# Optimization experiments

Measured on AMD Instinct MI355X. Metric: run time of the kernel, lower is better.

Reference implementation:

```python
import jax, jax.numpy as jnp
import numpy as np

N = 100000   # nodes
E = 1600000  # edges
DIM = 64
DIMS = [128, 64, 64, 64]  # [2*DIM] + 3*[DIM]
MAX_DEG = 64
NUM_LAB = 16

def _leaky(x):
    return jnp.where(x >= 0, x, 0.01 * x)

def _bn(x, g, b, eps=1e-5):
    # BatchNorm1d in training mode: per-feature batch mean / biased variance
    m = x.mean(axis=0)
    v = x.var(axis=0)
    return (x - m) * jax.lax.rsqrt(v + eps) * g + b

def setup_inputs() -> dict:
    key = jax.random.key(0)
    ks = jax.random.split(key, 40)
    d = {}
    d["node_deg"] = jax.random.randint(ks[0], (N,), 0, MAX_DEG + 1)
    d["node_lab"] = jax.random.randint(ks[1], (N,), 0, NUM_LAB)
    d["edge_index"] = jax.random.randint(ks[2], (2, E), 0, N)
    d["emb_deg"] = jax.random.normal(ks[3], (MAX_DEG + 1, DIM), jnp.float32) * 0.1
    d["emb_lab"] = jax.random.normal(ks[4], (NUM_LAB, DIM), jnp.float32) * 0.1
    k = 5
    for i, (n1, n2) in enumerate(zip(DIMS[:-1], DIMS[1:])):
        d[f"w{i}"] = jax.random.normal(ks[k], (n2, n1), jnp.float32) / np.sqrt(n1); k += 1
        d[f"b{i}"] = jnp.zeros((n2,), jnp.float32)
        d[f"g{i}"] = jnp.ones((n2,), jnp.float32)
        d[f"be{i}"] = jnp.zeros((n2,), jnp.float32)
    SUMD = sum(DIMS)  # 320
    d["fw1"] = jax.random.normal(ks[k], (DIM, SUMD), jnp.float32) / np.sqrt(SUMD); k += 1
    d["fb1"] = jnp.zeros((DIM,), jnp.float32)
    d["fg"] = jnp.ones((DIM,), jnp.float32)
    d["fbe"] = jnp.zeros((DIM,), jnp.float32)
    d["fw2"] = jax.random.normal(ks[k], (1, DIM), jnp.float32) / np.sqrt(DIM)
    d["fb2"] = jnp.zeros((1,), jnp.float32)
    return d

def reference(node_deg, node_lab, edge_index, emb_deg, emb_lab,
              w0, b0, g0, be0, w1, b1, g1, be1, w2, b2, g2, be2,
              fw1, fb1, fg, fbe, fw2, fb2):
    src, dst = edge_index[0], edge_index[1]
    # input embedding: concat of degree and label embeddings -> [N, 128]
    x0 = jnp.concatenate([emb_deg[node_deg], emb_lab[node_lab]], axis=1)
    z = [x0]
    for (w, b, g, be) in [(w0, b0, g0, be0), (w1, b1, g1, be1), (w2, b2, g2, be2)]:
        x = z[-1]
        # GINConv (eps=0): h = Linear(x + sum_{j in N(i)} x_j)
        agg = jax.ops.segment_sum(x[src], dst, num_segments=N)
        h = (x + agg) @ w.T + b
        z.append(_leaky(_bn(h, g, be)))
    xc = jnp.concatenate(z, axis=1)  # [N, 320]
    h = _leaky(_bn(xc @ fw1.T + fb1, fg, fbe))
    return jax.nn.sigmoid(h @ fw2.T + fb2).squeeze()  # [N]
```

## Files before the change

kernel.cpp:

```cpp
#include <hip/hip_runtime.h>
#include <math.h>

typedef __bf16 bf16;
typedef __attribute__((ext_vector_type(8))) __bf16 bf16x8;
typedef __attribute__((ext_vector_type(4))) float f32x4;

#define NBLK 128
#define NB_MAX 1600

__device__ __forceinline__ void bn_coeffs(const float* st, const float* g,
                                          const float* be, float inv_n, int d,
                                          float& sc, float& sh) {
  float mean = st[d] * inv_n;
  float var = st[64 + d] * inv_n - mean * mean;
  sc = g[d] * rsqrtf(var + 1e-5f);
  sh = be[d] - mean * sc;
}

__global__ __launch_bounds__(256) void bin_hist_kernel(const int* __restrict__ dst,
                                                       int* __restrict__ cnt,
                                                       int E, int ch, int nb) {
  __shared__ int lcnt[NB_MAX];
  int tid = threadIdx.x, blk = blockIdx.x;
  for (int t = tid; t < nb; t += 256) lcnt[t] = 0;
  __syncthreads();
  int base = blk * ch, eend = min(E, base + ch);
  for (int e = base + tid; e < eend; e += 256) atomicAdd(&lcnt[dst[e] >> 6], 1);
  __syncthreads();
  for (int t = tid; t < nb; t += 256) cnt[blk * nb + t] = lcnt[t];
}

__global__ __launch_bounds__(256) void bin_tot_kernel(const int* __restrict__ cnt,
                                                      int* __restrict__ tot, int nb) {
  int b = blockIdx.x * 256 + threadIdx.x;
  if (b >= nb) return;
  int s = 0;
  for (int blk = 0; blk < NBLK; ++blk) s += cnt[blk * nb + b];
  tot[b] = s;
}

__global__ __launch_bounds__(256) void scan_buckets_kernel(const int* __restrict__ tot,
                                                           int* __restrict__ bucketptr, int nb) {
  __shared__ int lds[256];
  int tid = threadIdx.x;
  const int CH = 7;
  int vals[CH];
  int s = 0;
#pragma unroll
  for (int k = 0; k < CH; ++k) {
    int i = tid * CH + k;
    vals[k] = (i < nb) ? tot[i] : 0;
    s += vals[k];
  }
  lds[tid] = s;
  __syncthreads();
  for (int off = 1; off < 256; off <<= 1) {
    int v = (tid >= off) ? lds[tid - off] : 0;
    __syncthreads();
    lds[tid] += v;
    __syncthreads();
  }
  int run = lds[tid] - s;
  if (tid == 0) bucketptr[0] = 0;
#pragma unroll
  for (int k = 0; k < CH; ++k) {
    int i = tid * CH + k;
    run += vals[k];
    if (i < nb) bucketptr[i + 1] = run;
  }
}

__global__ __launch_bounds__(256) void bin_off_kernel(const int* __restrict__ cnt,
                                                      const int* __restrict__ bucketptr,
                                                      int* __restrict__ woff, int nb) {
  int b = blockIdx.x * 256 + threadIdx.x;
  if (b >= nb) return;
  int run = bucketptr[b];
  for (int blk = 0; blk < NBLK; ++blk) {
    woff[blk * nb + b] = run;
    run += cnt[blk * nb + b];
  }
}

__global__ __launch_bounds__(256) void bin_scatter_kernel(const int* __restrict__ src,
                                                          const int* __restrict__ dst,
                                                          const int* __restrict__ woff,
                                                          int* __restrict__ packed,
                                                          int E, int ch, int nb) {
  __shared__ int cur[NB_MAX];
  int tid = threadIdx.x, blk = blockIdx.x;
  for (int t = tid; t < nb; t += 256) cur[t] = woff[blk * nb + t];
  __syncthreads();
  int base = blk * ch, eend = min(E, base + ch);
  for (int e = base + tid; e < eend; e += 256) {
    int d = dst[e], s = src[e];
    int pos = atomicAdd(&cur[d >> 6], 1);
    packed[pos] = ((d & 63) << 17) | s;
  }
}

__global__ __launch_bounds__(256) void csr_finalize_kernel(
    const int* __restrict__ packed, const int* __restrict__ bucketptr,
    int* __restrict__ rowptr, int* __restrict__ colidx, int n, int E) {
  __shared__ int hist[64], offs[64];
  int tid = threadIdx.x, b = blockIdx.x;
  if (tid < 64) hist[tid] = 0;
  __syncthreads();
  int beg = bucketptr[b], end = bucketptr[b + 1];
  for (int e = beg + tid; e < end; e += 256) atomicAdd(&hist[packed[e] >> 17], 1);
  __syncthreads();
  if (tid == 0) {
    int run = 0;
    for (int j = 0; j < 64; ++j) { offs[j] = run; run += hist[j]; }
  }
  __syncthreads();
  if (tid < 64) {
    int idx = b * 64 + tid;
    if (idx < n) rowptr[idx] = beg + offs[tid];
    hist[tid] = offs[tid];
  }
  if (b == 0 && tid == 64) rowptr[n] = E;
  __syncthreads();
  for (int e = beg + tid; e < end; e += 256) {
    int w = packed[e];
    int pos = atomicAdd(&hist[w >> 17], 1);
    colidx[beg + pos] = w & 0x1FFFF;
  }
}

__global__ __launch_bounds__(256) void mfma_gemm0(
    const int* __restrict__ deg, const int* __restrict__ lab,
    const float* __restrict__ ed, const float* __restrict__ el,
    const float* __restrict__ W, bf16* __restrict__ y, int n) {
  __shared__ bf16 As[64][136];
  __shared__ bf16 Bs[64][136];
  int tid = threadIdx.x;
  int nbase = blockIdx.x * 64;
  {
    int r = tid >> 2, c = tid & 3;
    int node = nbase + r;
    union { bf16 hh[32]; uint4 u[4]; } t;
    if (node < n) {
      int idx = (c < 2) ? deg[node] : lab[node];
      const float* srcp = (c < 2) ? (ed + (size_t)idx * 64 + c * 32)
                                  : (el + (size_t)idx * 64 + (c - 2) * 32);
#pragma unroll
      for (int j = 0; j < 8; ++j) {
        float4 f = ((const float4*)srcp)[j];
        t.hh[j * 4 + 0] = (bf16)f.x; t.hh[j * 4 + 1] = (bf16)f.y;
        t.hh[j * 4 + 2] = (bf16)f.z; t.hh[j * 4 + 3] = (bf16)f.w;
      }
    } else {
#pragma unroll
      for (int j = 0; j < 4; ++j) t.u[j] = uint4{0, 0, 0, 0};
    }
#pragma unroll
    for (int j = 0; j < 4; ++j) *(uint4*)&As[r][c * 32 + j * 8] = t.u[j];
    const float4* wp = (const float4*)(W + r * 128 + c * 32);
#pragma unroll
    for (int j = 0; j < 4; ++j) {
      float4 f0 = wp[j * 2], f1 = wp[j * 2 + 1];
      union { bf16 h[8]; uint4 u; } tw;
      tw.h[0] = (bf16)f0.x; tw.h[1] = (bf16)f0.y; tw.h[2] = (bf16)f0.z; tw.h[3] = (bf16)f0.w;
      tw.h[4] = (bf16)f1.x; tw.h[5] = (bf16)f1.y; tw.h[6] = (bf16)f1.z; tw.h[7] = (bf16)f1.w;
      *(uint4*)&Bs[r][c * 32 + j * 8] = tw.u;
    }
  }
  __syncthreads();
  int l = tid & 63, w = tid >> 6, m = l & 15, quad = l >> 4;
  f32x4 acc[4] = {{0.f, 0.f, 0.f, 0.f}, {0.f, 0.f, 0.f, 0.f},
                  {0.f, 0.f, 0.f, 0.f}, {0.f, 0.f, 0.f, 0.f}};
#pragma unroll
  for (int k0 = 0; k0 < 128; k0 += 32) {
    bf16x8 a = *(const bf16x8*)&As[w * 16 + m][k0 + quad * 8];
#pragma unroll
    for (int t = 0; t < 4; ++t) {
      bf16x8 b = *(const bf16x8*)&Bs[t * 16 + m][k0 + quad * 8];
      acc[t] = __builtin_amdgcn_mfma_f32_16x16x32_bf16(a, b, acc[t], 0, 0, 0);
    }
  }
#pragma unroll
  for (int t = 0; t < 4; ++t)
#pragma unroll
    for (int r4 = 0; r4 < 4; ++r4) {
      int node = nbase + w * 16 + quad * 4 + r4;
      if (node < n) y[(size_t)node * 64 + t * 16 + m] = (bf16)acc[t][r4];
    }
}

__global__ __launch_bounds__(256) void mfma_gemm_bn(
    const bf16* __restrict__ hin, const float* __restrict__ st,
    const float* __restrict__ g, const float* __restrict__ be, float inv_n,
    const float* __restrict__ W, bf16* __restrict__ z,
    bf16* __restrict__ y, int n) {
  __shared__ bf16 As[64][72];
  __shared__ bf16 Bs[64][72];
  __shared__ float ssc[64], ssh[64];
  int tid = threadIdx.x;
  int nbase = blockIdx.x * 64;
  if (tid < 64) {
    float sc, sh;
    bn_coeffs(st, g, be, inv_n, tid, sc, sh);
    ssc[tid] = sc; ssh[tid] = sh;
  }
  __syncthreads();
  {
    int r = tid >> 2, c = tid & 3;
    int node = nbase + r;
    union { bf16 h[16]; uint4 u[2]; } t;
    if (node < n) {
      const uint4* p = (const uint4*)(hin + (size_t)node * 64 + c * 16);
      union { uint4 u; bf16 h[8]; } a0, a1;
      a0.u = p[0]; a1.u = p[1];
#pragma unroll
      for (int j = 0; j < 8; ++j) {
        int d = c * 16 + j;
        float v = (float)a0.h[j] * ssc[d] + ssh[d];
        v = (v >= 0.f) ? v : 0.01f * v;
        t.h[j] = (bf16)v;
      }
#pragma unroll
      for (int j = 0; j < 8; ++j) {
        int d = c * 16 + 8 + j;
        float v = (float)a1.h[j] * ssc[d] + ssh[d];
        v = (v >= 0.f) ? v : 0.01f * v;
        t.h[8 + j] = (bf16)v;
      }
      *(uint4*)(z + (size_t)node * 64 + c * 16) = t.u[0];
      *(uint4*)(z + (size_t)node * 64 + c * 16 + 8) = t.u[1];
    } else {
      t.u[0] = uint4{0, 0, 0, 0}; t.u[1] = uint4{0, 0, 0, 0};
    }
    *(uint4*)&As[r][c * 16] = t.u[0];
    *(uint4*)&As[r][c * 16 + 8] = t.u[1];
    const float4* wp = (const float4*)(W + r * 64 + c * 16);
#pragma unroll
    for (int j = 0; j < 2; ++j) {
      float4 f0 = wp[j * 2], f1 = wp[j * 2 + 1];
      union { bf16 h[8]; uint4 u; } tw;
      tw.h[0] = (bf16)f0.x; tw.h[1] = (bf16)f0.y; tw.h[2] = (bf16)f0.z; tw.h[3] = (bf16)f0.w;
      tw.h[4] = (bf16)f1.x; tw.h[5] = (bf16)f1.y; tw.h[6] = (bf16)f1.z; tw.h[7] = (bf16)f1.w;
      *(uint4*)&Bs[r][c * 16 + j * 8] = tw.u;
    }
  }
  __syncthreads();
  int l = tid & 63, w = tid >> 6, m = l & 15, quad = l >> 4;
  f32x4 acc[4] = {{0.f, 0.f, 0.f, 0.f}, {0.f, 0.f, 0.f, 0.f},
                  {0.f, 0.f, 0.f, 0.f}, {0.f, 0.f, 0.f, 0.f}};
#pragma unroll
  for (int k0 = 0; k0 < 64; k0 += 32) {
    bf16x8 a = *(const bf16x8*)&As[w * 16 + m][k0 + quad * 8];
#pragma unroll
    for (int t = 0; t < 4; ++t) {
      bf16x8 b = *(const bf16x8*)&Bs[t * 16 + m][k0 + quad * 8];
      acc[t] = __builtin_amdgcn_mfma_f32_16x16x32_bf16(a, b, acc[t], 0, 0, 0);
    }
  }
#pragma unroll
  for (int t = 0; t < 4; ++t)
#pragma unroll
    for (int r4 = 0; r4 < 4; ++r4) {
      int node = nbase + w * 16 + quad * 4 + r4;
      if (node < n) y[(size_t)node * 64 + t * 16 + m] = (bf16)acc[t][r4];
    }
}

__global__ __launch_bounds__(256, 4) void gather_kernel(
    const bf16* __restrict__ y, const int* __restrict__ rowptr,
    const int* __restrict__ colidx, const float* __restrict__ bias,
    bf16* __restrict__ h, float* __restrict__ stats, int n) {
  __shared__ float s_sum[64], s_sq[64];
  int tid = threadIdx.x;
  if (tid < 64) { s_sum[tid] = 0.f; s_sq[tid] = 0.f; }
  __syncthreads();
  int lane = tid & 63, wv = tid >> 6;
  int g = lane >> 4, lh = lane & 15;
  const uint2* y2 = (const uint2*)y;
  uint2* h2 = (uint2*)h;
  float b0 = bias[4 * lh + 0], b1 = bias[4 * lh + 1];
  float b2 = bias[4 * lh + 2], b3 = bias[4 * lh + 3];
  float p0 = 0.f, p1 = 0.f, p2 = 0.f, p3 = 0.f;
  float q0 = 0.f, q1 = 0.f, q2 = 0.f, q3 = 0.f;
  int stride = gridDim.x * 16;

#define ACC4(d)                                                      \
  {                                                                  \
    union { unsigned u; float f; } t_;                               \
    t_.u = (d).x << 16;         a0 += t_.f;                          \
    t_.u = (d).x & 0xFFFF0000u; a1 += t_.f;                          \
    t_.u = (d).y << 16;         a2 += t_.f;                          \
    t_.u = (d).y & 0xFFFF0000u; a3 += t_.f;                          \
  }

  for (int nb = (blockIdx.x * 4 + wv) * 4; nb < n; nb += stride) {
    int node = nb + g;
    bool valid = node < n;
    int e = valid ? rowptr[node] : 0;
    int f = valid ? rowptr[node + 1] : 0;
    float a0 = 0.f, a1 = 0.f, a2 = 0.f, a3 = 0.f;
    for (;;) {
      bool a = (e + 8 <= f);
      if (__ballot(a) == 0ull) break;
      if (a) {
        int s0 = colidx[e + 0], s1 = colidx[e + 1], s2 = colidx[e + 2], s3 = colidx[e + 3];
        int s4 = colidx[e + 4], s5 = colidx[e + 5], s6 = colidx[e + 6], s7 = colidx[e + 7];
        uint2 d0 = y2[(size_t)s0 * 16 + lh];
        uint2 d1 = y2[(size_t)s1 * 16 + lh];
        uint2 d2 = y2[(size_t)s2 * 16 + lh];
        uint2 d3 = y2[(size_t)s3 * 16 + lh];
        uint2 d4 = y2[(size_t)s4 * 16 + lh];
        uint2 d5 = y2[(size_t)s5 * 16 + lh];
        uint2 d6 = y2[(size_t)s6 * 16 + lh];
        uint2 d7 = y2[(size_t)s7 * 16 + lh];
        ACC4(d0); ACC4(d1); ACC4(d2); ACC4(d3);
        ACC4(d4); ACC4(d5); ACC4(d6); ACC4(d7);
        e += 8;
      }
    }
    {
      bool a = (e + 4 <= f);
      if (__ballot(a) != 0ull) {
        if (a) {
          int s0 = colidx[e + 0], s1 = colidx[e + 1], s2 = colidx[e + 2], s3 = colidx[e + 3];
          uint2 d0 = y2[(size_t)s0 * 16 + lh];
          uint2 d1 = y2[(size_t)s1 * 16 + lh];
          uint2 d2 = y2[(size_t)s2 * 16 + lh];
          uint2 d3 = y2[(size_t)s3 * 16 + lh];
          ACC4(d0); ACC4(d1); ACC4(d2); ACC4(d3);
          e += 4;
        }
      }
    }
#pragma unroll
    for (int t = 0; t < 3; ++t) {
      bool a = e < f;
      if (a) {
        int s = colidx[e];
        uint2 d = y2[(size_t)s * 16 + lh];
        ACC4(d);
        ++e;
      }
    }
    if (valid) {
      uint2 sd = y2[(size_t)node * 16 + lh];
      float s0, s1, s2, s3;
      {
        union { unsigned u; float f; } t_;
        t_.u = sd.x << 16;         s0 = t_.f;
        t_.u = sd.x & 0xFFFF0000u; s1 = t_.f;
        t_.u = sd.y << 16;         s2 = t_.f;
        t_.u = sd.y & 0xFFFF0000u; s3 = t_.f;
      }
      float v0 = a0 + s0 + b0;
      float v1 = a1 + s1 + b1;
      float v2 = a2 + s2 + b2;
      float v3 = a3 + s3 + b3;
      union { bf16 hh[4]; uint2 u; } o;
      o.hh[0] = (bf16)v0; o.hh[1] = (bf16)v1;
      o.hh[2] = (bf16)v2; o.hh[3] = (bf16)v3;
      h2[(size_t)node * 16 + lh] = o.u;
      p0 += v0; q0 += v0 * v0;
      p1 += v1; q1 += v1 * v1;
      p2 += v2; q2 += v2 * v2;
      p3 += v3; q3 += v3 * v3;
    }
  }
#undef ACC4
  atomicAdd(&s_sum[4 * lh + 0], p0); atomicAdd(&s_sq[4 * lh + 0], q0);
  atomicAdd(&s_sum[4 * lh + 1], p1); atomicAdd(&s_sq[4 * lh + 1], q1);
  atomicAdd(&s_sum[4 * lh + 2], p2); atomicAdd(&s_sq[4 * lh + 2], q2);
  atomicAdd(&s_sum[4 * lh + 3], p3); atomicAdd(&s_sq[4 * lh + 3], q3);
  __syncthreads();
  if (tid < 64) {
    atomicAdd(&stats[tid], s_sum[tid]);
    atomicAdd(&stats[64 + tid], s_sq[tid]);
  }
}

__global__ __launch_bounds__(256) void mfma_final(
    const int* __restrict__ deg, const int* __restrict__ lab,
    const float* __restrict__ ed, const float* __restrict__ el,
    const bf16* __restrict__ z1, const bf16* __restrict__ z2,
    const bf16* __restrict__ h2, const float* __restrict__ st2,
    const float* __restrict__ g2, const float* __restrict__ be2, float inv_n,
    const float* __restrict__ fw1, const float* __restrict__ fb1,
    bf16* __restrict__ hf, float* __restrict__ stats, int n) {
  __shared__ bf16 As[64][136];
  __shared__ bf16 Bs[64][136];
  __shared__ float s_sum[64], s_sq[64], ssc[64], ssh[64];
  int tid = threadIdx.x;
  if (tid < 64) {
    s_sum[tid] = 0.f; s_sq[tid] = 0.f;
    float sc, sh;
    bn_coeffs(st2, g2, be2, inv_n, tid, sc, sh);
    ssc[tid] = sc; ssh[tid] = sh;
  }
  int nbase = blockIdx.x * 64;
  int l = tid & 63, w = tid >> 6, m = l & 15, quad = l >> 4;
  int r = tid >> 2, c = tid & 3;
  int node_r = nbase + r;
  f32x4 acc[4] = {{0.f, 0.f, 0.f, 0.f}, {0.f, 0.f, 0.f, 0.f},
                  {0.f, 0.f, 0.f, 0.f}, {0.f, 0.f, 0.f, 0.f}};

#pragma unroll
  for (int seg = 0; seg < 4; ++seg) {
    __syncthreads();
    if (seg == 0) {
      union { bf16 hh[32]; uint4 u[4]; } t;
      if (node_r < n) {
        int idx = (c < 2) ? deg[node_r] : lab[node_r];
        const float* srcp = (c < 2) ? (ed + (size_t)idx * 64 + c * 32)
                                    : (el + (size_t)idx * 64 + (c - 2) * 32);
#pragma unroll
        for (int j = 0; j < 8; ++j) {
          float4 f = ((const float4*)srcp)[j];
          t.hh[j * 4 + 0] = (bf16)f.x; t.hh[j * 4 + 1] = (bf16)f.y;
          t.hh[j * 4 + 2] = (bf16)f.z; t.hh[j * 4 + 3] = (bf16)f.w;
        }
      } else {
#pragma unroll
        for (int j = 0; j < 4; ++j) t.u[j] = uint4{0, 0, 0, 0};
      }
#pragma unroll
      for (int j = 0; j < 4; ++j) *(uint4*)&As[r][c * 32 + j * 8] = t.u[j];
      const float4* wp = (const float4*)(fw1 + r * 320 + c * 32);
#pragma unroll
      for (int j = 0; j < 4; ++j) {
        float4 f0 = wp[j * 2], f1 = wp[j * 2 + 1];
        union { bf16 h[8]; uint4 u; } tw;
        tw.h[0] = (bf16)f0.x; tw.h[1] = (bf16)f0.y; tw.h[2] = (bf16)f0.z; tw.h[3] = (bf16)f0.w;
        tw.h[4] = (bf16)f1.x; tw.h[5] = (bf16)f1.y; tw.h[6] = (bf16)f1.z; tw.h[7] = (bf16)f1.w;
        *(uint4*)&Bs[r][c * 32 + j * 8] = tw.u;
      }
    } else if (seg < 3) {
      const bf16* zz = (seg == 1) ? z1 : z2;
      uint4 v[2] = {};
      if (node_r < n) {
        const uint4* p = (const uint4*)(zz + (size_t)node_r * 64 + c * 16);
        v[0] = p[0]; v[1] = p[1];
      }
      *(uint4*)&As[r][c * 16] = v[0];
      *(uint4*)&As[r][c * 16 + 8] = v[1];
      const float4* wp = (const float4*)(fw1 + r * 320 + (seg == 1 ? 128 : 192) + c * 16);
#pragma unroll
      for (int j = 0; j < 2; ++j) {
        float4 f0 = wp[j * 2], f1 = wp[j * 2 + 1];
        union { bf16 h[8]; uint4 u; } t;
        t.h[0] = (bf16)f0.x; t.h[1] = (bf16)f0.y; t.h[2] = (bf16)f0.z; t.h[3] = (bf16)f0.w;
        t.h[4] = (bf16)f1.x; t.h[5] = (bf16)f1.y; t.h[6] = (bf16)f1.z; t.h[7] = (bf16)f1.w;
        *(uint4*)&Bs[r][c * 16 + j * 8] = t.u;
      }
    } else {
      union { bf16 h[16]; uint4 u[2]; } t;
      if (node_r < n) {
        const uint4* p = (const uint4*)(h2 + (size_t)node_r * 64 + c * 16);
        union { uint4 u; bf16 h[8]; } a0, a1;
        a0.u = p[0]; a1.u = p[1];
#pragma unroll
        for (int j = 0; j < 8; ++j) {
          int d = c * 16 + j;
          float v = (float)a0.h[j] * ssc[d] + ssh[d];
          v = (v >= 0.f) ? v : 0.01f * v;
          t.h[j] = (bf16)v;
        }
#pragma unroll
        for (int j = 0; j < 8; ++j) {
          int d = c * 16 + 8 + j;
          float v = (float)a1.h[j] * ssc[d] + ssh[d];
          v = (v >= 0.f) ? v : 0.01f * v;
          t.h[8 + j] = (bf16)v;
        }
      } else {
        t.u[0] = uint4{0, 0, 0, 0}; t.u[1] = uint4{0, 0, 0, 0};
      }
      *(uint4*)&As[r][c * 16] = t.u[0];
      *(uint4*)&As[r][c * 16 + 8] = t.u[1];
      const float4* wp = (const float4*)(fw1 + r * 320 + 256 + c * 16);
#pragma unroll
      for (int j = 0; j < 2; ++j) {
        float4 f0 = wp[j * 2], f1 = wp[j * 2 + 1];
        union { bf16 h[8]; uint4 u; } tw;
        tw.h[0] = (bf16)f0.x; tw.h[1] = (bf16)f0.y; tw.h[2] = (bf16)f0.z; tw.h[3] = (bf16)f0.w;
        tw.h[4] = (bf16)f1.x; tw.h[5] = (bf16)f1.y; tw.h[6] = (bf16)f1.z; tw.h[7] = (bf16)f1.w;
        *(uint4*)&Bs[r][c * 16 + j * 8] = tw.u;
      }
    }
    __syncthreads();
    int kmax = (seg == 0) ? 128 : 64;
    for (int k0 = 0; k0 < kmax; k0 += 32) {
      bf16x8 a = *(const bf16x8*)&As[w * 16 + m][k0 + quad * 8];
#pragma unroll
      for (int t = 0; t < 4; ++t) {
        bf16x8 b = *(const bf16x8*)&Bs[t * 16 + m][k0 + quad * 8];
        acc[t] = __builtin_amdgcn_mfma_f32_16x16x32_bf16(a, b, acc[t], 0, 0, 0);
      }
    }
  }

#pragma unroll
  for (int t = 0; t < 4; ++t) {
    int o = t * 16 + m;
    float bv = fb1[o];
    float s = 0.f, q = 0.f;
#pragma unroll
    for (int r4 = 0; r4 < 4; ++r4) {
      int node = nbase + w * 16 + quad * 4 + r4;
      if (node < n) {
        float v = acc[t][r4] + bv;
        hf[(size_t)node * 64 + o] = (bf16)v;
        s += v;
        q += v * v;
      }
    }
    atomicAdd(&s_sum[o], s);
    atomicAdd(&s_sq[o], q);
  }
  __syncthreads();
  if (tid < 64) {
    atomicAdd(&stats[tid], s_sum[tid]);
    atomicAdd(&stats[64 + tid], s_sq[tid]);
  }
}

__global__ __launch_bounds__(256) void final_out_kernel(
    const bf16* __restrict__ hf, const float* __restrict__ st,
    const float* __restrict__ g, const float* __restrict__ be, float inv_n,
    const float* __restrict__ fw2, const float* __restrict__ fb2,
    float* __restrict__ out, int n) {
  int lane = threadIdx.x & 63;
  int node = blockIdx.x * 4 + (threadIdx.x >> 6);
  if (node >= n) return;
  float sc, sh;
  bn_coeffs(st, g, be, inv_n, lane, sc, sh);
  float v = (float)hf[(size_t)node * 64 + lane] * sc + sh;
  v = (v >= 0.f) ? v : 0.01f * v;
  v *= fw2[lane];
#pragma unroll
  for (int off = 32; off > 0; off >>= 1) v += __shfl_xor(v, off);
  if (lane == 0) out[node] = 1.f / (1.f + expf(-(v + fb2[0])));
}

extern "C" void kernel_launch(void* const* d_in, const int* in_sizes, int n_in,
                              void* d_out, int out_size, void* d_ws, size_t ws_size,
                              hipStream_t stream) {
  const int* node_deg = (const int*)d_in[0];
  const int* node_lab = (const int*)d_in[1];
  const int* ei = (const int*)d_in[2];
  const float* emb_deg = (const float*)d_in[3];
  const float* emb_lab = (const float*)d_in[4];
  const float* w0 = (const float*)d_in[5];
  const float* b0 = (const float*)d_in[6];
  const float* g0 = (const float*)d_in[7];
  const float* be0 = (const float*)d_in[8];
  const float* w1 = (const float*)d_in[9];
  const float* b1 = (const float*)d_in[10];
  const float* g1 = (const float*)d_in[11];
  const float* be1 = (const float*)d_in[12];
  const float* w2 = (const float*)d_in[13];
  const float* b2 = (const float*)d_in[14];
  const float* g2 = (const float*)d_in[15];
  const float* be2 = (const float*)d_in[16];
  const float* fw1 = (const float*)d_in[17];
  const float* fb1 = (const float*)d_in[18];
  const float* fg = (const float*)d_in[19];
  const float* fbe = (const float*)d_in[20];
  const float* fw2 = (const float*)d_in[21];
  const float* fb2 = (const float*)d_in[22];

  const int N = in_sizes[0];
  const int E = in_sizes[2] / 2;
  const int* src = ei;
  const int* dst = ei + E;
  const int NB = (N + 63) >> 6;
  const int CH = (E + NBLK - 1) / NBLK;
  const float inv_n = 1.0f / N;

  char* ws = (char*)d_ws;
  size_t off = 0;
  auto alloc = [&](size_t bytes) {
    void* p = ws + off;
    off += (bytes + 255) & ~(size_t)255;
    return p;
  };
  bf16* z1 = (bf16*)alloc((size_t)N * 64 * 2);
  bf16* z2 = (bf16*)alloc((size_t)N * 64 * 2);
  bf16* h = (bf16*)alloc((size_t)N * 64 * 2);
  bf16* y = (bf16*)alloc((size_t)N * 64 * 2);
  int* packed = (int*)alloc((size_t)E * 4);
  int* colidx = (int*)alloc((size_t)E * 4);
  int* rowptr = (int*)alloc((size_t)(N + 1) * 4);
  int* cnt = (int*)alloc((size_t)NBLK * NB * 4);
  int* woff = (int*)alloc((size_t)NBLK * NB * 4);
  int* btot = (int*)alloc((size_t)NB * 4);
  int* bucketptr = (int*)alloc((size_t)(NB + 1) * 4);
  float* stats = (float*)alloc(4 * 256 * 4);

  hipMemsetAsync(stats, 0, 4 * 256 * 4, stream);

  bin_hist_kernel<<<NBLK, 256, 0, stream>>>(dst, cnt, E, CH, NB);
  bin_tot_kernel<<<(NB + 255) / 256, 256, 0, stream>>>(cnt, btot, NB);
  scan_buckets_kernel<<<1, 256, 0, stream>>>(btot, bucketptr, NB);
  bin_off_kernel<<<(NB + 255) / 256, 256, 0, stream>>>(cnt, bucketptr, woff, NB);
  bin_scatter_kernel<<<NBLK, 256, 0, stream>>>(src, dst, woff, packed, E, CH, NB);
  csr_finalize_kernel<<<NB, 256, 0, stream>>>(packed, bucketptr, rowptr, colidx, N, E);

  int ngrid = (N + 63) / 64;
  int ggrid = 2048;

  mfma_gemm0<<<ngrid, 256, 0, stream>>>(node_deg, node_lab, emb_deg, emb_lab, w0, y, N);
  gather_kernel<<<ggrid, 256, 0, stream>>>(y, rowptr, colidx, b0, h, stats, N);
  mfma_gemm_bn<<<ngrid, 256, 0, stream>>>(h, stats, g0, be0, inv_n, w1, z1, y, N);
  gather_kernel<<<ggrid, 256, 0, stream>>>(y, rowptr, colidx, b1, h, stats + 256, N);
  mfma_gemm_bn<<<ngrid, 256, 0, stream>>>(h, stats + 256, g1, be1, inv_n, w2, z2, y, N);
  gather_kernel<<<ggrid, 256, 0, stream>>>(y, rowptr, colidx, b2, h, stats + 512, N);
  mfma_final<<<ngrid, 256, 0, stream>>>(node_deg, node_lab, emb_deg, emb_lab, z1, z2, h,
                                        stats + 512, g2, be2, inv_n, fw1, fb1, y,
                                        stats + 768, N);
  final_out_kernel<<<(N + 3) / 4, 256, 0, stream>>>(y, stats + 768, fg, fbe, inv_n,
                                                    fw2, fb2, (float*)d_out, N);
}
```

Measured before the change: 530.9 us.

## Split CSR rows by source-node quarter and gather in tile-synchronised phases

The CSR finalize step now sorts each row's edges into four source-index ranges and records per-node split offsets. The gather kernel runs four phases, one per source quarter, so at any moment all waves read from roughly the same quarter of the feature table. The aim is better L2/MALL hit rates for the random neighbour reads. It also swaps the 2048-block grid-stride loop for one block per 64 nodes, with each 16-lane group handling four nodes two at a time and predicated 4-wide loads. The cost is an extra 1.6 MB splits array, more loop-control overhead, and loads wasted on small segments.

```diff
diff --git a/kernel.cpp b/kernel.cpp
--- a/kernel.cpp
+++ b/kernel.cpp
@@ -101,30 +101,43 @@
 
 __global__ __launch_bounds__(256) void csr_finalize_kernel(
     const int* __restrict__ packed, const int* __restrict__ bucketptr,
-    int* __restrict__ rowptr, int* __restrict__ colidx, int n, int E) {
-  __shared__ int hist[64], offs[64];
+    int* __restrict__ rowptr, int* __restrict__ colidx, int* __restrict__ splits,
+    int n, int E, int TN) {
+  __shared__ int hist[256], offs[256];
   int tid = threadIdx.x, b = blockIdx.x;
-  if (tid < 64) hist[tid] = 0;
+  hist[tid] = 0;
   __syncthreads();
   int beg = bucketptr[b], end = bucketptr[b + 1];
-  for (int e = beg + tid; e < end; e += 256) atomicAdd(&hist[packed[e] >> 17], 1);
+  for (int e = beg + tid; e < end; e += 256) {
+    int w = packed[e];
+    int s = w & 0x1FFFF;
+    int tile = (s >= TN) + (s >= 2 * TN) + (s >= 3 * TN);
+    atomicAdd(&hist[((w >> 17) << 2) + tile], 1);
+  }
   __syncthreads();
   if (tid == 0) {
     int run = 0;
-    for (int j = 0; j < 64; ++j) { offs[j] = run; run += hist[j]; }
-  }
-  __syncthreads();
+    for (int j = 0; j < 256; ++j) { offs[j] = run; run += hist[j]; }
+  }
+  __syncthreads();
+  {
+    int node = b * 64 + (tid >> 2);
+    if (node < n) splits[(size_t)node * 4 + (tid & 3)] = beg + offs[tid];
+  }
   if (tid < 64) {
     int idx = b * 64 + tid;
-    if (idx < n) rowptr[idx] = beg + offs[tid];
-    hist[tid] = offs[tid];
+    if (idx < n) rowptr[idx] = beg + offs[tid << 2];
   }
   if (b == 0 && tid == 64) rowptr[n] = E;
+  __syncthreads();
+  hist[tid] = offs[tid];
   __syncthreads();
   for (int e = beg + tid; e < end; e += 256) {
     int w = packed[e];
-    int pos = atomicAdd(&hist[w >> 17], 1);
-    colidx[beg + pos] = w & 0x1FFFF;
+    int s = w & 0x1FFFF;
+    int tile = (s >= TN) + (s >= 2 * TN) + (s >= 3 * TN);
+    int pos = atomicAdd(&hist[((w >> 17) << 2) + tile], 1);
+    colidx[beg + pos] = s;
   }
 }
 
@@ -267,81 +280,76 @@
 
 __global__ __launch_bounds__(256, 4) void gather_kernel(
     const bf16* __restrict__ y, const int* __restrict__ rowptr,
-    const int* __restrict__ colidx, const float* __restrict__ bias,
-    bf16* __restrict__ h, float* __restrict__ stats, int n) {
+    const int* __restrict__ splits, const int* __restrict__ colidx,
+    const float* __restrict__ bias, bf16* __restrict__ h,
+    float* __restrict__ stats, int n) {
   __shared__ float s_sum[64], s_sq[64];
   int tid = threadIdx.x;
   if (tid < 64) { s_sum[tid] = 0.f; s_sq[tid] = 0.f; }
   __syncthreads();
   int lane = tid & 63, wv = tid >> 6;
   int g = lane >> 4, lh = lane & 15;
+  int base = (blockIdx.x << 6) + (wv << 4) + (g << 2);
   const uint2* y2 = (const uint2*)y;
   uint2* h2 = (uint2*)h;
   float b0 = bias[4 * lh + 0], b1 = bias[4 * lh + 1];
   float b2 = bias[4 * lh + 2], b3 = bias[4 * lh + 3];
+  float acc[4][4];
+#pragma unroll
+  for (int j = 0; j < 4; ++j)
+#pragma unroll
+    for (int d = 0; d < 4; ++d) acc[j][d] = 0.f;
+
+#define ACCJ(j, d)                                                   \
+  {                                                                  \
+    union { unsigned u; float f; } t_;                               \
+    t_.u = (d).x << 16;         acc[j][0] += t_.f;                   \
+    t_.u = (d).x & 0xFFFF0000u; acc[j][1] += t_.f;                   \
+    t_.u = (d).y << 16;         acc[j][2] += t_.f;                   \
+    t_.u = (d).y & 0xFFFF0000u; acc[j][3] += t_.f;                   \
+  }
+
+#pragma unroll 1
+  for (int k = 0; k < 4; ++k) {
+#pragma unroll
+    for (int jp = 0; jp < 4; jp += 2) {
+      int nA = base + jp, nB = base + jp + 1;
+      bool vA = nA < n, vB = nB < n;
+      int eA = 0, fA = 0, eB = 0, fB = 0;
+      if (vA) {
+        eA = splits[(size_t)nA * 4 + k];
+        fA = (k == 3) ? rowptr[nA + 1] : splits[(size_t)nA * 4 + k + 1];
+      }
+      if (vB) {
+        eB = splits[(size_t)nB * 4 + k];
+        fB = (k == 3) ? rowptr[nB + 1] : splits[(size_t)nB * 4 + k + 1];
+      }
+      while (__ballot(eA < fA || eB < fB) != 0ull) {
+        uint2 dA0 = {0u, 0u}, dA1 = {0u, 0u}, dA2 = {0u, 0u}, dA3 = {0u, 0u};
+        uint2 dB0 = {0u, 0u}, dB1 = {0u, 0u}, dB2 = {0u, 0u}, dB3 = {0u, 0u};
+        if (eA + 0 < fA) { int s = colidx[eA + 0]; dA0 = y2[(size_t)s * 16 + lh]; }
+        if (eA + 1 < fA) { int s = colidx[eA + 1]; dA1 = y2[(size_t)s * 16 + lh]; }
+        if (eA + 2 < fA) { int s = colidx[eA + 2]; dA2 = y2[(size_t)s * 16 + lh]; }
+        if (eA + 3 < fA) { int s = colidx[eA + 3]; dA3 = y2[(size_t)s * 16 + lh]; }
+        if (eB + 0 < fB) { int s = colidx[eB + 0]; dB0 = y2[(size_t)s * 16 + lh]; }
+        if (eB + 1 < fB) { int s = colidx[eB + 1]; dB1 = y2[(size_t)s * 16 + lh]; }
+        if (eB + 2 < fB) { int s = colidx[eB + 2]; dB2 = y2[(size_t)s * 16 + lh]; }
+        if (eB + 3 < fB) { int s = colidx[eB + 3]; dB3 = y2[(size_t)s * 16 + lh]; }
+        ACCJ(jp, dA0); ACCJ(jp, dA1); ACCJ(jp, dA2); ACCJ(jp, dA3);
+        ACCJ(jp + 1, dB0); ACCJ(jp + 1, dB1); ACCJ(jp + 1, dB2); ACCJ(jp + 1, dB3);
+        eA = min(eA + 4, fA);
+        eB = min(eB + 4, fB);
+      }
+    }
+  }
+#undef ACCJ
+
   float p0 = 0.f, p1 = 0.f, p2 = 0.f, p3 = 0.f;
   float q0 = 0.f, q1 = 0.f, q2 = 0.f, q3 = 0.f;
-  int stride = gridDim.x * 16;
-
-#define ACC4(d)                                                      \
-  {                                                                  \
-    union { unsigned u; float f; } t_;                               \
-    t_.u = (d).x << 16;         a0 += t_.f;                          \
-    t_.u = (d).x & 0xFFFF0000u; a1 += t_.f;                          \
-    t_.u = (d).y << 16;         a2 += t_.f;                          \
-    t_.u = (d).y & 0xFFFF0000u; a3 += t_.f;                          \
-  }
-
-  for (int nb = (blockIdx.x * 4 + wv) * 4; nb < n; nb += stride) {
-    int node = nb + g;
-    bool valid = node < n;
-    int e = valid ? rowptr[node] : 0;
-    int f = valid ? rowptr[node + 1] : 0;
-    float a0 = 0.f, a1 = 0.f, a2 = 0.f, a3 = 0.f;
-    for (;;) {
-      bool a = (e + 8 <= f);
-      if (__ballot(a) == 0ull) break;
-      if (a) {
-        int s0 = colidx[e + 0], s1 = colidx[e + 1], s2 = colidx[e + 2], s3 = colidx[e + 3];
-        int s4 = colidx[e + 4], s5 = colidx[e + 5], s6 = colidx[e + 6], s7 = colidx[e + 7];
-        uint2 d0 = y2[(size_t)s0 * 16 + lh];
-        uint2 d1 = y2[(size_t)s1 * 16 + lh];
-        uint2 d2 = y2[(size_t)s2 * 16 + lh];
-        uint2 d3 = y2[(size_t)s3 * 16 + lh];
-        uint2 d4 = y2[(size_t)s4 * 16 + lh];
-        uint2 d5 = y2[(size_t)s5 * 16 + lh];
-        uint2 d6 = y2[(size_t)s6 * 16 + lh];
-        uint2 d7 = y2[(size_t)s7 * 16 + lh];
-        ACC4(d0); ACC4(d1); ACC4(d2); ACC4(d3);
-        ACC4(d4); ACC4(d5); ACC4(d6); ACC4(d7);
-        e += 8;
-      }
-    }
-    {
-      bool a = (e + 4 <= f);
-      if (__ballot(a) != 0ull) {
-        if (a) {
-          int s0 = colidx[e + 0], s1 = colidx[e + 1], s2 = colidx[e + 2], s3 = colidx[e + 3];
-          uint2 d0 = y2[(size_t)s0 * 16 + lh];
-          uint2 d1 = y2[(size_t)s1 * 16 + lh];
-          uint2 d2 = y2[(size_t)s2 * 16 + lh];
-          uint2 d3 = y2[(size_t)s3 * 16 + lh];
-          ACC4(d0); ACC4(d1); ACC4(d2); ACC4(d3);
-          e += 4;
-        }
-      }
-    }
-#pragma unroll
-    for (int t = 0; t < 3; ++t) {
-      bool a = e < f;
-      if (a) {
-        int s = colidx[e];
-        uint2 d = y2[(size_t)s * 16 + lh];
-        ACC4(d);
-        ++e;
-      }
-    }
-    if (valid) {
+#pragma unroll
+  for (int j = 0; j < 4; ++j) {
+    int node = base + j;
+    if (node < n) {
       uint2 sd = y2[(size_t)node * 16 + lh];
       float s0, s1, s2, s3;
       {
@@ -351,10 +359,10 @@
         t_.u = sd.y << 16;         s2 = t_.f;
         t_.u = sd.y & 0xFFFF0000u; s3 = t_.f;
       }
-      float v0 = a0 + s0 + b0;
-      float v1 = a1 + s1 + b1;
-      float v2 = a2 + s2 + b2;
-      float v3 = a3 + s3 + b3;
+      float v0 = acc[j][0] + s0 + b0;
+      float v1 = acc[j][1] + s1 + b1;
+      float v2 = acc[j][2] + s2 + b2;
+      float v3 = acc[j][3] + s3 + b3;
       union { bf16 hh[4]; uint2 u; } o;
       o.hh[0] = (bf16)v0; o.hh[1] = (bf16)v1;
       o.hh[2] = (bf16)v2; o.hh[3] = (bf16)v3;
@@ -365,7 +373,6 @@
       p3 += v3; q3 += v3 * v3;
     }
   }
-#undef ACC4
   atomicAdd(&s_sum[4 * lh + 0], p0); atomicAdd(&s_sq[4 * lh + 0], q0);
   atomicAdd(&s_sum[4 * lh + 1], p1); atomicAdd(&s_sq[4 * lh + 1], q1);
   atomicAdd(&s_sum[4 * lh + 2], p2); atomicAdd(&s_sq[4 * lh + 2], q2);
@@ -574,6 +581,7 @@
   const int NB = (N + 63) >> 6;
   const int CH = (E + NBLK - 1) / NBLK;
   const float inv_n = 1.0f / N;
+  const int TN = (N + 3) / 4;
 
   char* ws = (char*)d_ws;
   size_t off = 0;
@@ -589,6 +597,7 @@
   int* packed = (int*)alloc((size_t)E * 4);
   int* colidx = (int*)alloc((size_t)E * 4);
   int* rowptr = (int*)alloc((size_t)(N + 1) * 4);
+  int* splits = (int*)alloc((size_t)N * 4 * 4);
   int* cnt = (int*)alloc((size_t)NBLK * NB * 4);
   int* woff = (int*)alloc((size_t)NBLK * NB * 4);
   int* btot = (int*)alloc((size_t)NB * 4);
@@ -602,17 +611,17 @@
   scan_buckets_kernel<<<1, 256, 0, stream>>>(btot, bucketptr, NB);
   bin_off_kernel<<<(NB + 255) / 256, 256, 0, stream>>>(cnt, bucketptr, woff, NB);
   bin_scatter_kernel<<<NBLK, 256, 0, stream>>>(src, dst, woff, packed, E, CH, NB);
-  csr_finalize_kernel<<<NB, 256, 0, stream>>>(packed, bucketptr, rowptr, colidx, N, E);
+  csr_finalize_kernel<<<NB, 256, 0, stream>>>(packed, bucketptr, rowptr, colidx, splits,
+                                              N, E, TN);
 
   int ngrid = (N + 63) / 64;
-  int ggrid = 2048;
 
   mfma_gemm0<<<ngrid, 256, 0, stream>>>(node_deg, node_lab, emb_deg, emb_lab, w0, y, N);
-  gather_kernel<<<ggrid, 256, 0, stream>>>(y, rowptr, colidx, b0, h, stats, N);
+  gather_kernel<<<NB, 256, 0, stream>>>(y, rowptr, splits, colidx, b0, h, stats, N);
   mfma_gemm_bn<<<ngrid, 256, 0, stream>>>(h, stats, g0, be0, inv_n, w1, z1, y, N);
-  gather_kernel<<<ggrid, 256, 0, stream>>>(y, rowptr, colidx, b1, h, stats + 256, N);
+  gather_kernel<<<NB, 256, 0, stream>>>(y, rowptr, splits, colidx, b1, h, stats + 256, N);
   mfma_gemm_bn<<<ngrid, 256, 0, stream>>>(h, stats + 256, g1, be1, inv_n, w2, z2, y, N);
-  gather_kernel<<<ggrid, 256, 0, stream>>>(y, rowptr, colidx, b2, h, stats + 512, N);
+  gather_kernel<<<NB, 256, 0, stream>>>(y, rowptr, splits, colidx, b2, h, stats + 512, N);
   mfma_final<<<ngrid, 256, 0, stream>>>(node_deg, node_lab, emb_deg, emb_lab, z1, z2, h,
                                         stats + 512, g2, be2, inv_n, fw1, fb1, y,
                                         stats + 768, N);
```

Measured after the change: 668.5 us. 1.26x slower.
